# Optimization experiments

Measured on AMD Instinct MI355X. Metric: run time of the kernel, lower is better.

Reference implementation:

```python
import jax, jax.numpy as jnp
import numpy as np


def setup_inputs() -> dict:
    key = jax.random.key(0)
    ks = jax.random.split(key, 8)
    B, T, V, H, L = 64, 256, 32000, 512, 2
    in_tensor = jax.random.randint(ks[0], (B, T), 0, V)
    emb = jax.random.normal(ks[1], (V, H), dtype=jnp.float32) * 0.1
    emb = emb.at[0].set(0.0)  # padding_idx=0
    s = 1.0 / np.sqrt(H)
    wx = jax.random.normal(ks[2], (L, 4, H, H), dtype=jnp.float32) * s
    wh = jax.random.normal(ks[3], (L, 4, H, H), dtype=jnp.float32) * s
    bx = jnp.zeros((L, 4, H), dtype=jnp.float32)
    bh = jnp.zeros((L, 4, H), dtype=jnp.float32)
    wo = jax.random.normal(ks[4], (1, H), dtype=jnp.float32) * s
    bo = jnp.zeros((1,), dtype=jnp.float32)
    return {"in_tensor": in_tensor, "emb": emb, "wx": wx, "bx": bx,
            "wh": wh, "bh": bh, "wo": wo, "bo": bo}


def _block_lstm(x_btH, wx_l, bx_l, wh_l, bh_l, h0, c0):
    """Faithful BlockLSTM incl. the (o, c, h) -> (o, h, c) unpack bug:
    the carry swaps c_new into h-slot and h_new into c-slot each step,
    and the emitted sequence is the o-gate."""
    x_tbH = jnp.swapaxes(x_btH, 0, 1)  # [T,B,H]

    def step(carry, xt):
        h, c = carry
        # gates[k] = xt @ Wx[k].T + bx[k] + h @ Wh[k].T + bh[k], k in i,f,g,o
        g = (jnp.einsum('bh,koh->bko', xt, wx_l) + bx_l
             + jnp.einsum('bh,koh->bko', h, wh_l) + bh_l)
        i = jax.nn.sigmoid(g[:, 0])
        f = jax.nn.sigmoid(g[:, 1])
        gg = jnp.tanh(g[:, 2])
        o = jax.nn.sigmoid(g[:, 3])
        c_new = f * c + i * gg
        h_new = o * jnp.tanh(c_new)
        # bug: caller assigns h <- c_new, c <- h_new
        return (c_new, h_new), o

    (h_f, c_f), ys = jax.lax.scan(step, (h0, c0), x_tbH)
    return jnp.swapaxes(ys, 0, 1), h_f, c_f  # [B,T,H]


def reference(in_tensor, emb, wx, bx, wh, bh, wo, bo):
    B = in_tensor.shape[0]
    H = emb.shape[1]
    x = emb[in_tensor]  # [B,T,H]
    h = jnp.zeros((B, H), dtype=emb.dtype)
    c = jnp.zeros((B, H), dtype=emb.dtype)
    for l in range(wx.shape[0]):
        x, h, c = _block_lstm(x, wx[l], bx[l], wh[l], bh[l], h, c)
    pooled = jnp.mean(x, axis=1)  # [B,H]
    out = pooled @ wo.T + bo      # [B,1]
    return jax.nn.sigmoid(out)[:, 0]
```

## Files before the change

### kernel.cpp

```cpp
#include <hip/hip_runtime.h>

typedef __attribute__((ext_vector_type(8))) short short8;
typedef __attribute__((ext_vector_type(4))) float f32x4;
typedef unsigned short u16;
typedef unsigned int u32;
typedef unsigned long long u64;

#define T_LEN 256
#define XSTEP_U16 32768
#define CHUNK_U16 512
#define HSLOT_U64 8192

#define OFF_X0 0u
#define SZ_X0 (256u * 65536u)
#define OFF_Y0 (OFF_X0 + SZ_X0)
#define SZ_Y0 SZ_X0
#define OFF_HD (OFF_Y0 + SZ_Y0)
#define SZ_HD (4u * 2u * 65536u)
#define OFF_POOL (OFF_HD + SZ_HD)
#define SZ_POOL (512u * 64u * 4u)
#define OFF_YFLG (OFF_POOL + SZ_POOL)
#define SZ_YFLG (2u * 32u * 4u)

__device__ __forceinline__ u16 f2bf(float x) {
  unsigned u = __builtin_bit_cast(unsigned, x);
  return (u16)((u + 0x7fffu + ((u >> 16) & 1u)) >> 16);
}
__device__ __forceinline__ float sigf(float x) { return 1.f / (1.f + __expf(-x)); }
__device__ __forceinline__ float tanhfast(float x) {
  float e = __expf(2.f * x);
  return 1.f - 2.f / (e + 1.f);
}

__device__ __forceinline__ u64 ld8_llc(const u64* p) {
  return __hip_atomic_load(p, __ATOMIC_RELAXED, __HIP_MEMORY_SCOPE_AGENT);
}
__device__ __forceinline__ void st8_llc(u64* p, u64 v) {
  __hip_atomic_store(p, v, __ATOMIC_RELAXED, __HIP_MEMORY_SCOPE_AGENT);
}
__device__ __forceinline__ short8 ld16_llc(const u16* p) {
  const u64* q = (const u64*)p;
  u64 lo = ld8_llc(q), hi = ld8_llc(q + 1);
  union { u64 v[2]; short8 s; } u;
  u.v[0] = lo; u.v[1] = hi;
  return u.s;
}
__device__ __forceinline__ void st2_llc(u16* p, u16 v) {
  __hip_atomic_store(p, v, __ATOMIC_RELAXED, __HIP_MEMORY_SCOPE_AGENT);
}
__device__ __forceinline__ void st4_llc(u32* p, u32 v) {
  __hip_atomic_store(p, v, __ATOMIC_RELAXED, __HIP_MEMORY_SCOPE_AGENT);
}
__device__ __forceinline__ u32 ld4_llc(const u32* p) {
  return __hip_atomic_load(p, __ATOMIC_RELAXED, __HIP_MEMORY_SCOPE_AGENT);
}
__device__ __forceinline__ void poll_sc1(const u32* base, int lane, u32 tgt) {
  const u32* pf = base + (lane & 31);
  for (;;) {
    u32 v = ld4_llc(pf);
    if (__all((int)(v >= tgt))) break;
    __builtin_amdgcn_s_sleep(1);
  }
  asm volatile("" ::: "memory");
}

__device__ __forceinline__ short8 cvt8(const float* src) {
  float4 lo = *(const float4*)src;
  float4 hi = *(const float4*)(src + 4);
  short8 fr;
  fr[0] = (short)f2bf(lo.x); fr[1] = (short)f2bf(lo.y);
  fr[2] = (short)f2bf(lo.z); fr[3] = (short)f2bf(lo.w);
  fr[4] = (short)f2bf(hi.x); fr[5] = (short)f2bf(hi.y);
  fr[6] = (short)f2bf(hi.z); fr[7] = (short)f2bf(hi.w);
  return fr;
}

__global__ void gather_x0(const int* __restrict__ in_t, const float* __restrict__ emb,
                          u16* __restrict__ x0) {
  int gid = blockIdx.x * 256 + threadIdx.x;
  int c = gid >> 6, lane = gid & 63;
  int t = c >> 6, rem = c & 63;
  int kt = rem >> 2, nt = rem & 3;
  int b = nt * 16 + (lane & 15);
  int k0 = kt * 32 + ((lane >> 4) * 8);
  int row = in_t[b * T_LEN + t];
  *(short8*)(x0 + (size_t)c * CHUNK_U16 + lane * 8) =
      cvt8(emb + (size_t)row * 512 + k0);
}

__global__ __launch_bounds__(512, 1) void lstm_persist(
    const float* __restrict__ wx, const float* __restrict__ bx,
    const float* __restrict__ wh, const float* __restrict__ bh,
    const u16* __restrict__ x0, u16* __restrict__ y0,
    u16* __restrict__ hd, float* __restrict__ pool, u32* __restrict__ yflg) {
  __shared__ float part[8][64][32];

  const int tid = threadIdx.x;
  const int w = tid >> 6, lane = tid & 63;
  const int q = lane >> 4, col = lane & 15;
  const int bid = blockIdx.x;
  const int g = bid & 3;
  const int layer = g >> 1, sb = g & 1;
  const int u = bid >> 2;
  const bool xside = (w < 4);

  short8 af[4][8];
  {
    const int gt_a = col & 3, hsub = col >> 2;
#pragma unroll
    for (int mt = 0; mt < 4; ++mt) {
      const int h_out = u * 16 + mt * 4 + hsub;
      if (xside) {
        const float* wrow = wx + ((size_t)(layer * 4 + gt_a) * 512 + h_out) * 512;
#pragma unroll
        for (int ks = 0; ks < 4; ++ks)
          af[mt][ks] = cvt8(wrow + (w * 4 + ks) * 32 + q * 8);
      } else {
        const float* wrow = wh + ((size_t)(layer * 4 + gt_a) * 512 + h_out) * 512;
        const int e = w - 4;
#pragma unroll
        for (int ks = 0; ks < 8; ++ks) {
          const int ktg = e * 8 + ks;
          const int hb = 16 * ktg + 4 * q;
          short8 fr;
          fr[0] = (short)f2bf(wrow[hb + 0]);
          fr[1] = (short)f2bf(wrow[hb + 1]);
          fr[2] = 0; fr[3] = 0;
          fr[4] = (short)f2bf(wrow[hb + 2]);
          fr[5] = (short)f2bf(wrow[hb + 3]);
          fr[6] = 0; fr[7] = 0;
          af[mt][ks] = fr;
        }
      }
    }
  }

  const int hl = tid >> 5, n = tid & 31;
  const int h_g = u * 16 + hl;
  float bias[4];
#pragma unroll
  for (int r = 0; r < 4; ++r)
    bias[r] = bx[(layer * 4 + r) * 512 + h_g] + bh[(layer * 4 + r) * 512 + h_g];
  const size_t offY = ((size_t)((h_g >> 5) * 4 + sb * 2 + (n >> 4)) * 64 +
                       (n & 15) + 16 * ((h_g >> 3) & 3)) * 8 + (h_g & 7);
  const size_t hoff = ((size_t)(4 * u + (w >> 1)) * 32 + n) * 2 + (w & 1);

  const u16* xbase = layer ? y0 : x0;
  u64* hdl = (u64*)hd + (size_t)g * 2 * HSLOT_U64;
  u32* yf_own = yflg + sb * 32 + u;
  const u32* yf_grp = yflg + sb * 32;

  float cst = 0.f, opool = 0.f;

  for (int t = 0; t < T_LEN; ++t) {
    f32x4 acc[4][2] = {};
    if (xside) {
      if (layer == 1) poll_sc1(yf_grp, lane, (u32)(t + 1));
      const u16* xs = xbase + (size_t)t * XSTEP_U16;
#pragma unroll
      for (int ks = 0; ks < 4; ++ks) {
        const int ktl = w * 4 + ks;
        const u16* p = xs + ((size_t)(ktl * 4 + 2 * sb) * 64 + lane) * 8;
        short8 f0, f1;
        if (layer == 0) {
          f0 = *(const short8*)p;
          f1 = *(const short8*)(p + CHUNK_U16);
        } else {
          f0 = ld16_llc(p);
          f1 = ld16_llc(p + CHUNK_U16);
        }
#pragma unroll
        for (int mt = 0; mt < 4; ++mt) {
          acc[mt][0] = __builtin_amdgcn_mfma_f32_16x16x32_bf16(af[mt][ks], f0,
                                                               acc[mt][0], 0, 0, 0);
          acc[mt][1] = __builtin_amdgcn_mfma_f32_16x16x32_bf16(af[mt][ks], f1,
                                                               acc[mt][1], 0, 0, 0);
        }
      }
    } else {
      const int e = w - 4;
      const u64* hs = hdl + (size_t)(t & 1) * HSLOT_U64;
      const u32 tagv = (u32)t;
#pragma unroll
      for (int c = 0; c < 2; ++c) {
        u64 d0[4], d1[4], d2[4], d3[4];
        for (;;) {
#pragma unroll
          for (int ks4 = 0; ks4 < 4; ++ks4) {
            const int ktg = e * 8 + c * 4 + ks4;
            const u64* p0 = hs + ((size_t)((4 * ktg + q) * 32 + col)) * 2;
            const u64* p1 = hs + ((size_t)((4 * ktg + q) * 32 + 16 + col)) * 2;
            d0[ks4] = ld8_llc(p0); d1[ks4] = ld8_llc(p0 + 1);
            d2[ks4] = ld8_llc(p1); d3[ks4] = ld8_llc(p1 + 1);
          }
          int ok = 1;
#pragma unroll
          for (int ks4 = 0; ks4 < 4; ++ks4)
            ok &= (int)(((u32)(d0[ks4] >> 32) == tagv) &
                        ((u32)(d1[ks4] >> 32) == tagv) &
                        ((u32)(d2[ks4] >> 32) == tagv) &
                        ((u32)(d3[ks4] >> 32) == tagv));
          if (__all(ok)) break;
          __builtin_amdgcn_s_sleep(1);
        }
#pragma unroll
        for (int ks4 = 0; ks4 < 4; ++ks4) {
          union { u64 v[2]; short8 s; } ua, ub;
          ua.v[0] = d0[ks4]; ua.v[1] = d1[ks4];
          ub.v[0] = d2[ks4]; ub.v[1] = d3[ks4];
#pragma unroll
          for (int mt = 0; mt < 4; ++mt) {
            acc[mt][0] = __builtin_amdgcn_mfma_f32_16x16x32_bf16(
                af[mt][c * 4 + ks4], ua.s, acc[mt][0], 0, 0, 0);
            acc[mt][1] = __builtin_amdgcn_mfma_f32_16x16x32_bf16(
                af[mt][c * 4 + ks4], ub.s, acc[mt][1], 0, 0, 0);
          }
        }
      }
    }
#pragma unroll
    for (int mt = 0; mt < 4; ++mt)
#pragma unroll
      for (int ntl = 0; ntl < 2; ++ntl)
#pragma unroll
        for (int r = 0; r < 4; ++r)
          part[w][mt * 16 + q * 4 + r][ntl * 16 + col] = acc[mt][ntl][r];
    __syncthreads();

    if (layer == 0) {
      asm volatile("s_waitcnt vmcnt(0)" ::: "memory");
      __syncthreads();
      if (tid == 1) st4_llc(yf_own, (u32)t);
    }

    float v[4];
#pragma unroll
    for (int gt = 0; gt < 4; ++gt) {
      float s = 0.f;
#pragma unroll
      for (int ww = 0; ww < 8; ++ww) s += part[ww][4 * hl + gt][n];
      v[gt] = s + bias[gt];
    }
    const float ig = sigf(v[0]);
    const float fg = sigf(v[1]);
    const float gg = tanhfast(v[2]);
    const float og = sigf(v[3]);
    const float cn = fg * cst + ig * gg;
    const float hn = og * tanhfast(cn);
    cst = hn;
    const float pcn = __shfl_xor(cn, 32, 64);
    {
      u64* hdst = hdl + (size_t)((t + 1) & 1) * HSLOT_U64;
      if (lane < 32) {
        u64 val = (u64)(u16)f2bf(cn) | ((u64)(u16)f2bf(pcn) << 16) |
                  ((u64)(u32)(t + 1) << 32);
        st8_llc(hdst + hoff, val);
      }
    }
    if (layer == 0) {
      st2_llc(y0 + (size_t)t * XSTEP_U16 + offY, f2bf(og));
    } else {
      opool += og;
    }
    __syncthreads();
  }

  if (layer == 0) {
    asm volatile("s_waitcnt vmcnt(0)" ::: "memory");
    __syncthreads();
    if (tid == 1) st4_llc(yf_own, (u32)T_LEN);
  } else {
    pool[(size_t)h_g * 64 + sb * 32 + n] = opool;
  }
}

__global__ void finalize_k(const float* __restrict__ pool, const float* __restrict__ wo,
                           const float* __restrict__ bo, float* __restrict__ out) {
  const int b = threadIdx.x;
  float s = 0.f;
  for (int h = 0; h < 512; ++h) s += pool[h * 64 + b] * wo[h];
  out[b] = sigf(s * (1.f / 256.f) + bo[0]);
}

extern "C" void kernel_launch(void* const* d_in, const int* in_sizes, int n_in,
                              void* d_out, int out_size, void* d_ws, size_t ws_size,
                              hipStream_t stream) {
  const int* in_t = (const int*)d_in[0];
  const float* emb = (const float*)d_in[1];
  const float* wx = (const float*)d_in[2];
  const float* bx = (const float*)d_in[3];
  const float* wh = (const float*)d_in[4];
  const float* bh = (const float*)d_in[5];
  const float* wo = (const float*)d_in[6];
  const float* bo = (const float*)d_in[7];
  float* out = (float*)d_out;
  char* ws = (char*)d_ws;
  u16* x0 = (u16*)(ws + OFF_X0);
  u16* y0 = (u16*)(ws + OFF_Y0);
  u16* hd = (u16*)(ws + OFF_HD);
  float* pool = (float*)(ws + OFF_POOL);
  u32* yflg = (u32*)(ws + OFF_YFLG);

  hipMemsetAsync(ws + OFF_HD, 0, SZ_HD, stream);
  hipMemsetAsync(ws + OFF_YFLG, 0, SZ_YFLG, stream);
  gather_x0<<<4096, 256, 0, stream>>>(in_t, emb, x0);
  lstm_persist<<<128, 512, 0, stream>>>(wx, bx, wh, bh, x0, y0, hd, pool, yflg);
  finalize_k<<<1, 64, 0, stream>>>(pool, wo, bo, out);
}
```

Baseline: 817.4 us.

## Halve persistent LSTM grid, give each block 32 hidden units

The persistent LSTM kernel now runs on 64 blocks instead of 128. Each block owns 32 hidden units, with 8 M-tiles per wave instead of 4. The recurrent weight fragments switch from a half-zero packed layout to dense K=32 fragments, so the h-side does half as many MFMAs per unit of work. The x-side and h-side waves now accumulate into a shared 4-slot partial buffer, which adds an extra barrier. Fewer blocks means fewer spin-polling participants and less cross-block flag and h traffic per step, at the cost of more serial work per block and higher register pressure.

```diff
diff --git a/kernel.cpp b/kernel.cpp
--- a/kernel.cpp
+++ b/kernel.cpp
@@ -20,7 +20,7 @@
 #define OFF_POOL (OFF_HD + SZ_HD)
 #define SZ_POOL (512u * 64u * 4u)
 #define OFF_YFLG (OFF_POOL + SZ_POOL)
-#define SZ_YFLG (2u * 32u * 4u)
+#define SZ_YFLG (2u * 16u * 4u)
 
 __device__ __forceinline__ u16 f2bf(float x) {
   unsigned u = __builtin_bit_cast(unsigned, x);
@@ -55,7 +55,7 @@
   return __hip_atomic_load(p, __ATOMIC_RELAXED, __HIP_MEMORY_SCOPE_AGENT);
 }
 __device__ __forceinline__ void poll_sc1(const u32* base, int lane, u32 tgt) {
-  const u32* pf = base + (lane & 31);
+  const u32* pf = base + (lane & 15);
   for (;;) {
     u32 v = ld4_llc(pf);
     if (__all((int)(v >= tgt))) break;
@@ -93,7 +93,7 @@
     const float* __restrict__ wh, const float* __restrict__ bh,
     const u16* __restrict__ x0, u16* __restrict__ y0,
     u16* __restrict__ hd, float* __restrict__ pool, u32* __restrict__ yflg) {
-  __shared__ float part[8][64][32];
+  __shared__ float part[4][128][32];
 
   const int tid = threadIdx.x;
   const int w = tid >> 6, lane = tid & 63;
@@ -103,63 +103,53 @@
   const int layer = g >> 1, sb = g & 1;
   const int u = bid >> 2;
   const bool xside = (w < 4);
-
-  short8 af[4][8];
+  const int e = w & 3;
+
+  short8 af[8][4];
   {
     const int gt_a = col & 3, hsub = col >> 2;
-#pragma unroll
-    for (int mt = 0; mt < 4; ++mt) {
-      const int h_out = u * 16 + mt * 4 + hsub;
-      if (xside) {
-        const float* wrow = wx + ((size_t)(layer * 4 + gt_a) * 512 + h_out) * 512;
-#pragma unroll
-        for (int ks = 0; ks < 4; ++ks)
-          af[mt][ks] = cvt8(wrow + (w * 4 + ks) * 32 + q * 8);
-      } else {
-        const float* wrow = wh + ((size_t)(layer * 4 + gt_a) * 512 + h_out) * 512;
-        const int e = w - 4;
-#pragma unroll
-        for (int ks = 0; ks < 8; ++ks) {
-          const int ktg = e * 8 + ks;
-          const int hb = 16 * ktg + 4 * q;
-          short8 fr;
-          fr[0] = (short)f2bf(wrow[hb + 0]);
-          fr[1] = (short)f2bf(wrow[hb + 1]);
-          fr[2] = 0; fr[3] = 0;
-          fr[4] = (short)f2bf(wrow[hb + 2]);
-          fr[5] = (short)f2bf(wrow[hb + 3]);
-          fr[6] = 0; fr[7] = 0;
-          af[mt][ks] = fr;
-        }
-      }
+    const float* wsel = xside ? wx : wh;
+#pragma unroll
+    for (int mt = 0; mt < 8; ++mt) {
+      const int h_out = u * 32 + mt * 4 + hsub;
+      const float* wrow = wsel + ((size_t)(layer * 4 + gt_a) * 512 + h_out) * 512;
+#pragma unroll
+      for (int ks = 0; ks < 4; ++ks)
+        af[mt][ks] = cvt8(wrow + (e * 4 + ks) * 32 + q * 8);
     }
   }
 
   const int hl = tid >> 5, n = tid & 31;
-  const int h_g = u * 16 + hl;
-  float bias[4];
-#pragma unroll
-  for (int r = 0; r < 4; ++r)
-    bias[r] = bx[(layer * 4 + r) * 512 + h_g] + bh[(layer * 4 + r) * 512 + h_g];
-  const size_t offY = ((size_t)((h_g >> 5) * 4 + sb * 2 + (n >> 4)) * 64 +
-                       (n & 15) + 16 * ((h_g >> 3) & 3)) * 8 + (h_g & 7);
-  const size_t hoff = ((size_t)(4 * u + (w >> 1)) * 32 + n) * 2 + (w & 1);
+  float bias[2][4];
+  size_t offY[2], hoff[2];
+  const int a2 = hl >> 1;
+#pragma unroll
+  for (int P = 0; P < 2; ++P) {
+    const int h_g = u * 32 + hl + 16 * P;
+#pragma unroll
+    for (int r = 0; r < 4; ++r)
+      bias[P][r] = bx[(layer * 4 + r) * 512 + h_g] + bh[(layer * 4 + r) * 512 + h_g];
+    offY[P] = ((size_t)((h_g >> 5) * 4 + sb * 2 + (n >> 4)) * 64 +
+               (n & 15) + 16 * ((h_g >> 3) & 3)) * 8 + (h_g & 7);
+    hoff[P] = ((size_t)(8 * u + 4 * P + (a2 >> 1)) * 32 + n) * 2 + (a2 & 1);
+  }
 
   const u16* xbase = layer ? y0 : x0;
   u64* hdl = (u64*)hd + (size_t)g * 2 * HSLOT_U64;
-  u32* yf_own = yflg + sb * 32 + u;
-  const u32* yf_grp = yflg + sb * 32;
-
-  float cst = 0.f, opool = 0.f;
+  u32* yf_own = yflg + sb * 16 + u;
+  const u32* yf_grp = yflg + sb * 16;
+
+  float cst[2] = {0.f, 0.f};
+  float opool[2] = {0.f, 0.f};
 
   for (int t = 0; t < T_LEN; ++t) {
-    f32x4 acc[4][2] = {};
+    f32x4 acc[8][2] = {};
     if (xside) {
       if (layer == 1) poll_sc1(yf_grp, lane, (u32)(t + 1));
       const u16* xs = xbase + (size_t)t * XSTEP_U16;
 #pragma unroll
       for (int ks = 0; ks < 4; ++ks) {
-        const int ktl = w * 4 + ks;
+        const int ktl = e * 4 + ks;
         const u16* p = xs + ((size_t)(ktl * 4 + 2 * sb) * 64 + lane) * 8;
         short8 f0, f1;
         if (layer == 0) {
@@ -170,61 +160,72 @@
           f1 = ld16_llc(p + CHUNK_U16);
         }
 #pragma unroll
-        for (int mt = 0; mt < 4; ++mt) {
+        for (int mt = 0; mt < 8; ++mt) {
           acc[mt][0] = __builtin_amdgcn_mfma_f32_16x16x32_bf16(af[mt][ks], f0,
                                                                acc[mt][0], 0, 0, 0);
           acc[mt][1] = __builtin_amdgcn_mfma_f32_16x16x32_bf16(af[mt][ks], f1,
                                                                acc[mt][1], 0, 0, 0);
         }
       }
+#pragma unroll
+      for (int mt = 0; mt < 8; ++mt)
+#pragma unroll
+        for (int ntl = 0; ntl < 2; ++ntl)
+#pragma unroll
+          for (int r = 0; r < 4; ++r)
+            part[w][mt * 16 + q * 4 + r][ntl * 16 + col] = acc[mt][ntl][r];
     } else {
-      const int e = w - 4;
       const u64* hs = hdl + (size_t)(t & 1) * HSLOT_U64;
       const u32 tagv = (u32)t;
-#pragma unroll
-      for (int c = 0; c < 2; ++c) {
-        u64 d0[4], d1[4], d2[4], d3[4];
-        for (;;) {
-#pragma unroll
-          for (int ks4 = 0; ks4 < 4; ++ks4) {
-            const int ktg = e * 8 + c * 4 + ks4;
-            const u64* p0 = hs + ((size_t)((4 * ktg + q) * 32 + col)) * 2;
-            const u64* p1 = hs + ((size_t)((4 * ktg + q) * 32 + 16 + col)) * 2;
-            d0[ks4] = ld8_llc(p0); d1[ks4] = ld8_llc(p0 + 1);
-            d2[ks4] = ld8_llc(p1); d3[ks4] = ld8_llc(p1 + 1);
-          }
-          int ok = 1;
-#pragma unroll
-          for (int ks4 = 0; ks4 < 4; ++ks4)
-            ok &= (int)(((u32)(d0[ks4] >> 32) == tagv) &
-                        ((u32)(d1[ks4] >> 32) == tagv) &
-                        ((u32)(d2[ks4] >> 32) == tagv) &
-                        ((u32)(d3[ks4] >> 32) == tagv));
-          if (__all(ok)) break;
-          __builtin_amdgcn_s_sleep(1);
-        }
-#pragma unroll
-        for (int ks4 = 0; ks4 < 4; ++ks4) {
-          union { u64 v[2]; short8 s; } ua, ub;
-          ua.v[0] = d0[ks4]; ua.v[1] = d1[ks4];
-          ub.v[0] = d2[ks4]; ub.v[1] = d3[ks4];
-#pragma unroll
-          for (int mt = 0; mt < 4; ++mt) {
-            acc[mt][0] = __builtin_amdgcn_mfma_f32_16x16x32_bf16(
-                af[mt][c * 4 + ks4], ua.s, acc[mt][0], 0, 0, 0);
-            acc[mt][1] = __builtin_amdgcn_mfma_f32_16x16x32_bf16(
-                af[mt][c * 4 + ks4], ub.s, acc[mt][1], 0, 0, 0);
+      u64 dd[4][2][4];
+      for (;;) {
+#pragma unroll
+        for (int kr = 0; kr < 4; ++kr) {
+#pragma unroll
+          for (int ntl = 0; ntl < 2; ++ntl) {
+            const int Qp0 = (e * 4 + kr) * 8 + 2 * q;
+            const u64* b0 = hs + ((size_t)Qp0 * 32 + ntl * 16 + col) * 2;
+            dd[kr][ntl][0] = ld8_llc(b0);
+            dd[kr][ntl][1] = ld8_llc(b0 + 1);
+            dd[kr][ntl][2] = ld8_llc(b0 + 64);
+            dd[kr][ntl][3] = ld8_llc(b0 + 65);
           }
         }
-      }
-    }
-#pragma unroll
-    for (int mt = 0; mt < 4; ++mt)
-#pragma unroll
-      for (int ntl = 0; ntl < 2; ++ntl)
-#pragma unroll
-        for (int r = 0; r < 4; ++r)
-          part[w][mt * 16 + q * 4 + r][ntl * 16 + col] = acc[mt][ntl][r];
+        int ok = 1;
+#pragma unroll
+        for (int kr = 0; kr < 4; ++kr)
+#pragma unroll
+          for (int ntl = 0; ntl < 2; ++ntl)
+#pragma unroll
+            for (int j = 0; j < 4; ++j)
+              ok &= (int)((u32)(dd[kr][ntl][j] >> 32) == tagv);
+        if (__all(ok)) break;
+        __builtin_amdgcn_s_sleep(1);
+      }
+#pragma unroll
+      for (int kr = 0; kr < 4; ++kr) {
+#pragma unroll
+        for (int ntl = 0; ntl < 2; ++ntl) {
+          union { u64 v[2]; short8 s; } uf;
+          uf.v[0] = (u64)(u32)dd[kr][ntl][0] | ((u64)(u32)dd[kr][ntl][1] << 32);
+          uf.v[1] = (u64)(u32)dd[kr][ntl][2] | ((u64)(u32)dd[kr][ntl][3] << 32);
+#pragma unroll
+          for (int mt = 0; mt < 8; ++mt)
+            acc[mt][ntl] = __builtin_amdgcn_mfma_f32_16x16x32_bf16(
+                af[mt][kr], uf.s, acc[mt][ntl], 0, 0, 0);
+        }
+      }
+    }
+    __syncthreads();
+    if (!xside) {
+#pragma unroll
+      for (int mt = 0; mt < 8; ++mt)
+#pragma unroll
+        for (int ntl = 0; ntl < 2; ++ntl)
+#pragma unroll
+          for (int r = 0; r < 4; ++r)
+            part[e][mt * 16 + q * 4 + r][ntl * 16 + col] += acc[mt][ntl][r];
+    }
     __syncthreads();
 
     if (layer == 0) {
@@ -233,34 +234,34 @@
       if (tid == 1) st4_llc(yf_own, (u32)t);
     }
 
-    float v[4];
-#pragma unroll
-    for (int gt = 0; gt < 4; ++gt) {
-      float s = 0.f;
-#pragma unroll
-      for (int ww = 0; ww < 8; ++ww) s += part[ww][4 * hl + gt][n];
-      v[gt] = s + bias[gt];
-    }
-    const float ig = sigf(v[0]);
-    const float fg = sigf(v[1]);
-    const float gg = tanhfast(v[2]);
-    const float og = sigf(v[3]);
-    const float cn = fg * cst + ig * gg;
-    const float hn = og * tanhfast(cn);
-    cst = hn;
-    const float pcn = __shfl_xor(cn, 32, 64);
-    {
-      u64* hdst = hdl + (size_t)((t + 1) & 1) * HSLOT_U64;
-      if (lane < 32) {
+    u64* hdst = hdl + (size_t)((t + 1) & 1) * HSLOT_U64;
+    u16* ydst = y0 + (size_t)t * XSTEP_U16;
+#pragma unroll
+    for (int P = 0; P < 2; ++P) {
+      const int row0 = 4 * (hl + 16 * P);
+      float v[4];
+#pragma unroll
+      for (int gt = 0; gt < 4; ++gt)
+        v[gt] = part[0][row0 + gt][n] + part[1][row0 + gt][n] +
+                part[2][row0 + gt][n] + part[3][row0 + gt][n] + bias[P][gt];
+      const float ig = sigf(v[0]);
+      const float fg = sigf(v[1]);
+      const float gg = tanhfast(v[2]);
+      const float og = sigf(v[3]);
+      const float cn = fg * cst[P] + ig * gg;
+      const float hn = og * tanhfast(cn);
+      cst[P] = hn;
+      const float pcn = __shfl_xor(cn, 32, 64);
+      if ((hl & 1) == 0) {
         u64 val = (u64)(u16)f2bf(cn) | ((u64)(u16)f2bf(pcn) << 16) |
                   ((u64)(u32)(t + 1) << 32);
-        st8_llc(hdst + hoff, val);
-      }
-    }
-    if (layer == 0) {
-      st2_llc(y0 + (size_t)t * XSTEP_U16 + offY, f2bf(og));
-    } else {
-      opool += og;
+        st8_llc(hdst + hoff[P], val);
+      }
+      if (layer == 0) {
+        st2_llc(ydst + offY[P], f2bf(og));
+      } else {
+        opool[P] += og;
+      }
     }
     __syncthreads();
   }
@@ -270,7 +271,9 @@
     __syncthreads();
     if (tid == 1) st4_llc(yf_own, (u32)T_LEN);
   } else {
-    pool[(size_t)h_g * 64 + sb * 32 + n] = opool;
+#pragma unroll
+    for (int P = 0; P < 2; ++P)
+      pool[(size_t)(u * 32 + hl + 16 * P) * 64 + sb * 32 + n] = opool[P];
   }
 }
 
@@ -304,6 +307,6 @@
   hipMemsetAsync(ws + OFF_HD, 0, SZ_HD, stream);
   hipMemsetAsync(ws + OFF_YFLG, 0, SZ_YFLG, stream);
   gather_x0<<<4096, 256, 0, stream>>>(in_t, emb, x0);
-  lstm_persist<<<128, 512, 0, stream>>>(wx, bx, wh, bh, x0, y0, hd, pool, yflg);
+  lstm_persist<<<64, 512, 0, stream>>>(wx, bx, wh, bh, x0, y0, hd, pool, yflg);
   finalize_k<<<1, 64, 0, stream>>>(pool, wo, bo, out);
 }
```

Result: slower. 1.592 ms (+94.8%).
